# Kernel tuning notes

Hardware: AMD Instinct MI355X
Metric: run time of the kernel (lower is better)

## Reference

```python
import jax, jax.numpy as jnp
import numpy as np

B, K, D, C = 8192, 16, 1024, 512


def setup_inputs() -> dict:
    key = jax.random.key(0)
    k1, k2, k3, k4, k5 = jax.random.split(key, 5)
    concepts = jax.random.normal(k1, (B, K, D), dtype=jnp.float32)
    slot_ids = jax.random.randint(k2, (B,), 0, K)
    labels = jax.random.randint(k3, (B,), 0, C)
    # per-slot Linear(concept_dim -> num_classes): weight (K, C, D), bias (K, C)
    W = jax.random.normal(k4, (K, C, D), dtype=jnp.float32) / np.sqrt(D).astype(np.float32)
    bias = jax.random.normal(k5, (K, C), dtype=jnp.float32) * 0.01
    return {"concepts": concepts, "slot_ids": slot_ids, "labels": labels, "W": W, "bias": bias}


def reference(concepts, slot_ids, labels, W, bias):
    # Each example b uses slot s=slot_ids[b]: logits = concepts[b, s, :] @ W[s].T + bias[s].
    # Vectorized as K batched GEMMs over the slot axis, then gather the relevant row.
    logits = jnp.einsum('bkd,kcd->bkc', concepts, W) + bias  # (B, K, C)
    logp = jax.nn.log_softmax(logits, axis=-1)
    bidx = jnp.arange(concepts.shape[0])
    ce = -logp[bidx, slot_ids, labels]  # per-example cross entropy (B,)
    nK = W.shape[0]
    counts = jax.ops.segment_sum(jnp.ones_like(ce), slot_ids, num_segments=nK)
    sums = jax.ops.segment_sum(ce, slot_ids, num_segments=nK)
    means = sums / jnp.maximum(counts, 1.0)          # per-slot mean CE (= F.cross_entropy per group)
    present = counts > 0
    n_present = jnp.maximum(jnp.sum(present), 1)     # torch: count of unique slots, max(count,1)
    return jnp.sum(jnp.where(present, means, 0.0)) / n_present
```

## Files before the change

### kernel.cpp

```cpp
#include <hip/hip_runtime.h>
#include <hip/hip_bf16.h>

#define B_N 8192
#define K_N 16
#define D_N 1024
#define C_N 512
#define BM  32

typedef __bf16 bf16x8 __attribute__((ext_vector_type(8)));
typedef float  f32x4  __attribute__((ext_vector_type(4)));
typedef float  f32x4v __attribute__((ext_vector_type(4)));
typedef unsigned int u32x4 __attribute__((ext_vector_type(4)));

static __device__ __forceinline__ unsigned short f2bf(float f) {
    union { float f; unsigned int u; } x; x.f = f;
    unsigned int r = x.u + 0x7FFFu + ((x.u >> 16) & 1u);
    return (unsigned short)(r >> 16);
}

static __device__ __forceinline__ bf16x8 load_bf8(const unsigned short* p) {
    union { u32x4 u; bf16x8 v; } t;
    t.u = *(const u32x4*)p;
    return t.v;
}

static __device__ __forceinline__ bf16x8 zero_bf8() {
    union { u32x4 u; bf16x8 v; } t;
    u32x4 z = {0u, 0u, 0u, 0u};
    t.u = z;
    return t.v;
}

__global__ __launch_bounds__(256) void prep(const int* __restrict__ slot_ids,
                                            const int* __restrict__ labels,
                                            int* __restrict__ counts,
                                            int* __restrict__ offsets_g,
                                            float* __restrict__ ce_sums,
                                            int* __restrict__ order_rows,
                                            int* __restrict__ lab_g) {
    __shared__ int h[256][K_N];
    __shared__ int g[256][K_N];
    __shared__ int soff[K_N];
    int t = threadIdx.x;
    int ids[32];

#pragma unroll
    for (int s = 0; s < K_N; ++s) h[t][s] = 0;
#pragma unroll
    for (int i = 0; i < 32; ++i) {
        int b = i * 256 + t;
        int s = slot_ids[b];
        ids[i] = s;
        h[t][s]++;
    }
#pragma unroll
    for (int s = 0; s < K_N; ++s) g[t][s] = h[t][s];
    __syncthreads();

    for (int d = 1; d < 256; d <<= 1) {
        int v[K_N];
        if (t >= d) {
#pragma unroll
            for (int s = 0; s < K_N; ++s) v[s] = h[t - d][s];
        }
        __syncthreads();
        if (t >= d) {
#pragma unroll
            for (int s = 0; s < K_N; ++s) h[t][s] += v[s];
        }
        __syncthreads();
    }

    if (t == 0) {
        int a = 0;
#pragma unroll
        for (int s = 0; s < K_N; ++s) {
            int c = h[255][s];
            counts[s] = c;
            soff[s] = a;
            offsets_g[s] = a;
            a += c;
        }
    }
    if (t < K_N) ce_sums[t] = 0.f;
    __syncthreads();

#pragma unroll
    for (int s = 0; s < K_N; ++s) h[t][s] = soff[s] + h[t][s] - g[t][s];

#pragma unroll
    for (int i = 0; i < 32; ++i) {
        int b = i * 256 + t;
        int s = ids[i];
        int idx = h[t][s]++;
        order_rows[idx] = b * K_N + s;
        lab_g[idx] = labels[b];
    }
}

__global__ void convw(const float* __restrict__ W, unsigned short* __restrict__ Wb) {
    int i = (blockIdx.x * 256 + threadIdx.x) * 8;
    f32x4v a = *(const f32x4v*)(W + i);
    f32x4v b = *(const f32x4v*)(W + i + 4);
    u32x4 o;
    o[0] = (unsigned)f2bf(a[0]) | ((unsigned)f2bf(a[1]) << 16);
    o[1] = (unsigned)f2bf(a[2]) | ((unsigned)f2bf(a[3]) << 16);
    o[2] = (unsigned)f2bf(b[0]) | ((unsigned)f2bf(b[1]) << 16);
    o[3] = (unsigned)f2bf(b[2]) | ((unsigned)f2bf(b[3]) << 16);
    *(u32x4*)(Wb + i) = o;
}

__global__ __launch_bounds__(256) void gemm_ce(
        const float* __restrict__ concepts, const unsigned short* __restrict__ Wb,
        const float* __restrict__ bias, const int* __restrict__ counts,
        const int* __restrict__ offsets, const int* __restrict__ order_rows,
        const int* __restrict__ lab_g, float* __restrict__ ce_sums) {
    int s = blockIdx.y;
    int cnt = counts[s];
    int row0 = blockIdx.x * BM;
    if (row0 >= cnt) return;
    int nrows = min(BM, cnt - row0);
    int base = offsets[s];

    int tid = threadIdx.x;
    int wave = tid >> 6, lane = tid & 63;
    int col = lane & 15, quad = lane >> 4;
    int c0 = wave * 128;

    __shared__ int srow[BM];
    if (tid < BM)
        srow[tid] = order_rows[base + row0 + min(tid, nrows - 1)];
    __syncthreads();

    f32x4 acc[2][8];
    f32x4 zf = {0.f, 0.f, 0.f, 0.f};
#pragma unroll
    for (int m = 0; m < 2; ++m)
#pragma unroll
        for (int t = 0; t < 8; ++t) acc[m][t] = zf;

    const float* aptr[2];
    bool avalid[2];
#pragma unroll
    for (int m = 0; m < 2; ++m) {
        int lr = m * 16 + col;
        avalid[m] = lr < nrows;
        aptr[m] = concepts + (size_t)srow[lr] * D_N + quad * 8;
    }
    const unsigned short* bptr = Wb + ((size_t)s * C_N + c0 + col) * D_N + quad * 8;

    for (int k = 0; k < D_N; k += 32) {
        bf16x8 af[2];
#pragma unroll
        for (int m = 0; m < 2; ++m) {
            f32x4 a0 = *(const f32x4*)(aptr[m] + k);
            f32x4 a1 = *(const f32x4*)(aptr[m] + k + 4);
            bf16x8 v;
            v[0] = (__bf16)a0[0]; v[1] = (__bf16)a0[1];
            v[2] = (__bf16)a0[2]; v[3] = (__bf16)a0[3];
            v[4] = (__bf16)a1[0]; v[5] = (__bf16)a1[1];
            v[6] = (__bf16)a1[2]; v[7] = (__bf16)a1[3];
            af[m] = avalid[m] ? v : zero_bf8();
        }
        bf16x8 bfr[8];
#pragma unroll
        for (int t = 0; t < 8; ++t)
            bfr[t] = load_bf8(bptr + (size_t)t * 16 * D_N + k);
#pragma unroll
        for (int m = 0; m < 2; ++m)
#pragma unroll
            for (int t = 0; t < 8; ++t)
                acc[m][t] = __builtin_amdgcn_mfma_f32_16x16x32_bf16(af[m], bfr[t], acc[m][t], 0, 0, 0);
    }

    __shared__ float smax[4][BM];
    __shared__ float ssum[4][BM];
    __shared__ float gmax[BM];
    __shared__ float slab[BM];

#pragma unroll
    for (int t = 0; t < 8; ++t) {
        float bv = bias[(size_t)s * C_N + c0 + t * 16 + col];
#pragma unroll
        for (int m = 0; m < 2; ++m)
#pragma unroll
            for (int r = 0; r < 4; ++r) acc[m][t][r] += bv;
    }

#pragma unroll
    for (int m = 0; m < 2; ++m)
#pragma unroll
        for (int r = 0; r < 4; ++r) {
            float v = acc[m][0][r];
#pragma unroll
            for (int t = 1; t < 8; ++t) v = fmaxf(v, acc[m][t][r]);
            v = fmaxf(v, __shfl_xor(v, 1, 64));
            v = fmaxf(v, __shfl_xor(v, 2, 64));
            v = fmaxf(v, __shfl_xor(v, 4, 64));
            v = fmaxf(v, __shfl_xor(v, 8, 64));
            if (col == 0) smax[wave][m * 16 + quad * 4 + r] = v;
        }
    __syncthreads();
    if (tid < BM)
        gmax[tid] = fmaxf(fmaxf(smax[0][tid], smax[1][tid]),
                          fmaxf(smax[2][tid], smax[3][tid]));
    __syncthreads();

#pragma unroll
    for (int m = 0; m < 2; ++m)
#pragma unroll
        for (int r = 0; r < 4; ++r) {
            int row = m * 16 + quad * 4 + r;
            float gm = gmax[row];
            int lab = (row < nrows) ? lab_g[base + row0 + row] : -1;
            float sv = 0.f;
#pragma unroll
            for (int t = 0; t < 8; ++t) {
                float x = acc[m][t][r];
                sv += __expf(x - gm);
                if (c0 + t * 16 + col == lab) slab[row] = x;
            }
            sv += __shfl_xor(sv, 1, 64);
            sv += __shfl_xor(sv, 2, 64);
            sv += __shfl_xor(sv, 4, 64);
            sv += __shfl_xor(sv, 8, 64);
            if (col == 0) ssum[wave][row] = sv;
        }
    __syncthreads();

    if (wave == 0) {
        float ce = 0.f;
        if (lane < nrows) {
            float gs = ssum[0][lane] + ssum[1][lane] + ssum[2][lane] + ssum[3][lane];
            ce = gmax[lane] + __logf(gs) - slab[lane];
        }
        ce += __shfl_xor(ce, 1, 64);
        ce += __shfl_xor(ce, 2, 64);
        ce += __shfl_xor(ce, 4, 64);
        ce += __shfl_xor(ce, 8, 64);
        ce += __shfl_xor(ce, 16, 64);
        ce += __shfl_xor(ce, 32, 64);
        if (lane == 0) atomicAdd(&ce_sums[s], ce);
    }
}

__global__ void finalize(const int* __restrict__ counts, const float* __restrict__ ce_sums,
                         float* __restrict__ out) {
    if (threadIdx.x == 0 && blockIdx.x == 0) {
        float tot = 0.f; int np = 0;
        for (int s = 0; s < K_N; ++s) {
            int c = counts[s];
            if (c > 0) { tot += ce_sums[s] / (float)c; np++; }
        }
        out[0] = tot / (float)(np > 0 ? np : 1);
    }
}

extern "C" void kernel_launch(void* const* d_in, const int* in_sizes, int n_in,
                              void* d_out, int out_size, void* d_ws, size_t ws_size,
                              hipStream_t stream) {
    const float* concepts = (const float*)d_in[0];
    const int*   slot_ids = (const int*)d_in[1];
    const int*   labels   = (const int*)d_in[2];
    const float* W        = (const float*)d_in[3];
    const float* bias     = (const float*)d_in[4];
    float* out = (float*)d_out;

    char* ws = (char*)d_ws;
    int*   counts     = (int*)(ws + 0);
    int*   offsets    = (int*)(ws + 64);
    float* ce_sums    = (float*)(ws + 192);
    int*   order_rows = (int*)(ws + 256);
    int*   lab_g      = (int*)(ws + 256 + 4 * B_N);
    unsigned short* Wb = (unsigned short*)(ws + 131072);

    convw<<<(K_N * C_N * D_N) / (256 * 8), 256, 0, stream>>>(W, Wb);
    prep<<<1, 256, 0, stream>>>(slot_ids, labels, counts, offsets, ce_sums, order_rows, lab_g);
    gemm_ce<<<dim3(B_N / BM, K_N), 256, 0, stream>>>(concepts, Wb, bias, counts, offsets,
                                                     order_rows, lab_g, ce_sums);
    finalize<<<1, 1, 0, stream>>>(counts, ce_sums, out);
}
```

Measured before the change: 750.6 us.

## Use compact 1D slot-block grid, halve row tile, fuse setup and finalize

Merges the weight conversion and the slot histogram/sort into one launch, and folds the final reduction into the GEMM kernel through a last-block-done atomic counter. The GEMM grid changes from a sparse (B/BM, K) grid, where most blocks exit early, to a compact 1D list of per-slot blocks found via prefix block bases. BM drops from 32 to 16, so each block does one MFMA row tile and there are more blocks. This removes launch overhead and idle blocks, but each block now reuses every bf16 weight fragment it loads for half as many rows.

Result: faster. 733.6 us (-2.3%).

```diff
diff --git a/kernel.cpp b/kernel.cpp
--- a/kernel.cpp
+++ b/kernel.cpp
@@ -5,11 +5,12 @@
 #define K_N 16
 #define D_N 1024
 #define C_N 512
-#define BM  32
+#define BM  16
+#define CONVW_BLOCKS ((K_N * C_N * D_N) / (256 * 8))
+#define GEMM_BLOCKS  (B_N / BM + K_N)
 
 typedef __bf16 bf16x8 __attribute__((ext_vector_type(8)));
 typedef float  f32x4  __attribute__((ext_vector_type(4)));
-typedef float  f32x4v __attribute__((ext_vector_type(4)));
 typedef unsigned int u32x4 __attribute__((ext_vector_type(4)));
 
 static __device__ __forceinline__ unsigned short f2bf(float f) {
@@ -31,18 +32,32 @@
     return t.v;
 }
 
-__global__ __launch_bounds__(256) void prep(const int* __restrict__ slot_ids,
-                                            const int* __restrict__ labels,
-                                            int* __restrict__ counts,
-                                            int* __restrict__ offsets_g,
-                                            float* __restrict__ ce_sums,
-                                            int* __restrict__ order_rows,
-                                            int* __restrict__ lab_g) {
+__global__ __launch_bounds__(256) void setup(
+        const float* __restrict__ W, unsigned short* __restrict__ Wb,
+        const int* __restrict__ slot_ids, const int* __restrict__ labels,
+        int* __restrict__ counts, int* __restrict__ offsets_g,
+        int* __restrict__ blk_base, int* __restrict__ done,
+        float* __restrict__ ce_sums, int* __restrict__ order_rows,
+        int* __restrict__ lab_g) {
     __shared__ int h[256][K_N];
-    __shared__ int g[256][K_N];
     __shared__ int soff[K_N];
     int t = threadIdx.x;
+
+    if (blockIdx.x < CONVW_BLOCKS) {
+        size_t i = ((size_t)blockIdx.x * 256 + t) * 8;
+        f32x4 a = *(const f32x4*)(W + i);
+        f32x4 b = *(const f32x4*)(W + i + 4);
+        u32x4 o;
+        o[0] = (unsigned)f2bf(a[0]) | ((unsigned)f2bf(a[1]) << 16);
+        o[1] = (unsigned)f2bf(a[2]) | ((unsigned)f2bf(a[3]) << 16);
+        o[2] = (unsigned)f2bf(b[0]) | ((unsigned)f2bf(b[1]) << 16);
+        o[3] = (unsigned)f2bf(b[2]) | ((unsigned)f2bf(b[3]) << 16);
+        *(u32x4*)(Wb + i) = o;
+        return;
+    }
+
     int ids[32];
+    int own[K_N];
 
 #pragma unroll
     for (int s = 0; s < K_N; ++s) h[t][s] = 0;
@@ -54,7 +69,7 @@
         h[t][s]++;
     }
 #pragma unroll
-    for (int s = 0; s < K_N; ++s) g[t][s] = h[t][s];
+    for (int s = 0; s < K_N; ++s) own[s] = h[t][s];
     __syncthreads();
 
     for (int d = 1; d < 256; d <<= 1) {
@@ -72,7 +87,8 @@
     }
 
     if (t == 0) {
-        int a = 0;
+        int a = 0, nb = 0;
+        blk_base[0] = 0;
 #pragma unroll
         for (int s = 0; s < K_N; ++s) {
             int c = h[255][s];
@@ -80,145 +96,123 @@
             soff[s] = a;
             offsets_g[s] = a;
             a += c;
-        }
+            nb += (c + BM - 1) / BM;
+            blk_base[s + 1] = nb;
+        }
+        *done = 0;
     }
     if (t < K_N) ce_sums[t] = 0.f;
     __syncthreads();
 
 #pragma unroll
-    for (int s = 0; s < K_N; ++s) h[t][s] = soff[s] + h[t][s] - g[t][s];
+    for (int s = 0; s < K_N; ++s) own[s] = soff[s] + h[t][s] - own[s];
 
 #pragma unroll
     for (int i = 0; i < 32; ++i) {
         int b = i * 256 + t;
         int s = ids[i];
-        int idx = h[t][s]++;
+        int idx = own[s]++;
         order_rows[idx] = b * K_N + s;
         lab_g[idx] = labels[b];
     }
-}
-
-__global__ void convw(const float* __restrict__ W, unsigned short* __restrict__ Wb) {
-    int i = (blockIdx.x * 256 + threadIdx.x) * 8;
-    f32x4v a = *(const f32x4v*)(W + i);
-    f32x4v b = *(const f32x4v*)(W + i + 4);
-    u32x4 o;
-    o[0] = (unsigned)f2bf(a[0]) | ((unsigned)f2bf(a[1]) << 16);
-    o[1] = (unsigned)f2bf(a[2]) | ((unsigned)f2bf(a[3]) << 16);
-    o[2] = (unsigned)f2bf(b[0]) | ((unsigned)f2bf(b[1]) << 16);
-    o[3] = (unsigned)f2bf(b[2]) | ((unsigned)f2bf(b[3]) << 16);
-    *(u32x4*)(Wb + i) = o;
 }
 
 __global__ __launch_bounds__(256) void gemm_ce(
         const float* __restrict__ concepts, const unsigned short* __restrict__ Wb,
         const float* __restrict__ bias, const int* __restrict__ counts,
-        const int* __restrict__ offsets, const int* __restrict__ order_rows,
-        const int* __restrict__ lab_g, float* __restrict__ ce_sums) {
-    int s = blockIdx.y;
-    int cnt = counts[s];
-    int row0 = blockIdx.x * BM;
-    if (row0 >= cnt) return;
-    int nrows = min(BM, cnt - row0);
-    int base = offsets[s];
-
+        const int* __restrict__ offsets, const int* __restrict__ blk_base,
+        const int* __restrict__ order_rows, const int* __restrict__ lab_g,
+        int* __restrict__ done, float* __restrict__ ce_sums,
+        float* __restrict__ out) {
+    __shared__ int srow[BM];
+    __shared__ float smax[4][BM];
+    __shared__ float ssum[4][BM];
+    __shared__ float gmax[BM];
+    __shared__ float slab[BM];
+
+    int bid = blockIdx.x;
+    int nb_total = blk_base[K_N];
     int tid = threadIdx.x;
-    int wave = tid >> 6, lane = tid & 63;
-    int col = lane & 15, quad = lane >> 4;
-    int c0 = wave * 128;
-
-    __shared__ int srow[BM];
-    if (tid < BM)
-        srow[tid] = order_rows[base + row0 + min(tid, nrows - 1)];
-    __syncthreads();
-
-    f32x4 acc[2][8];
-    f32x4 zf = {0.f, 0.f, 0.f, 0.f};
-#pragma unroll
-    for (int m = 0; m < 2; ++m)
-#pragma unroll
-        for (int t = 0; t < 8; ++t) acc[m][t] = zf;
-
-    const float* aptr[2];
-    bool avalid[2];
-#pragma unroll
-    for (int m = 0; m < 2; ++m) {
-        int lr = m * 16 + col;
-        avalid[m] = lr < nrows;
-        aptr[m] = concepts + (size_t)srow[lr] * D_N + quad * 8;
-    }
-    const unsigned short* bptr = Wb + ((size_t)s * C_N + c0 + col) * D_N + quad * 8;
-
-    for (int k = 0; k < D_N; k += 32) {
-        bf16x8 af[2];
-#pragma unroll
-        for (int m = 0; m < 2; ++m) {
-            f32x4 a0 = *(const f32x4*)(aptr[m] + k);
-            f32x4 a1 = *(const f32x4*)(aptr[m] + k + 4);
+
+    if (bid < nb_total) {
+        int s = 0;
+        while (s < K_N - 1 && bid >= blk_base[s + 1]) ++s;
+        int cnt = counts[s];
+        int base = offsets[s];
+        int row0 = (bid - blk_base[s]) * BM;
+        int nrows = min(BM, cnt - row0);
+
+        int wave = tid >> 6, lane = tid & 63;
+        int col = lane & 15, quad = lane >> 4;
+        int c0 = wave * 128;
+
+        if (tid < BM)
+            srow[tid] = order_rows[base + row0 + min(tid, nrows - 1)];
+        __syncthreads();
+
+        f32x4 acc[8];
+        f32x4 zf = {0.f, 0.f, 0.f, 0.f};
+#pragma unroll
+        for (int t8 = 0; t8 < 8; ++t8) acc[t8] = zf;
+
+        bool avalid = col < nrows;
+        const float* aptr = concepts + (size_t)srow[col] * D_N + quad * 8;
+        const unsigned short* bptr = Wb + ((size_t)s * C_N + c0 + col) * D_N + quad * 8;
+
+        for (int k = 0; k < D_N; k += 32) {
+            f32x4 a0 = *(const f32x4*)(aptr + k);
+            f32x4 a1 = *(const f32x4*)(aptr + k + 4);
             bf16x8 v;
             v[0] = (__bf16)a0[0]; v[1] = (__bf16)a0[1];
             v[2] = (__bf16)a0[2]; v[3] = (__bf16)a0[3];
             v[4] = (__bf16)a1[0]; v[5] = (__bf16)a1[1];
             v[6] = (__bf16)a1[2]; v[7] = (__bf16)a1[3];
-            af[m] = avalid[m] ? v : zero_bf8();
-        }
-        bf16x8 bfr[8];
-#pragma unroll
-        for (int t = 0; t < 8; ++t)
-            bfr[t] = load_bf8(bptr + (size_t)t * 16 * D_N + k);
-#pragma unroll
-        for (int m = 0; m < 2; ++m)
-#pragma unroll
-            for (int t = 0; t < 8; ++t)
-                acc[m][t] = __builtin_amdgcn_mfma_f32_16x16x32_bf16(af[m], bfr[t], acc[m][t], 0, 0, 0);
-    }
-
-    __shared__ float smax[4][BM];
-    __shared__ float ssum[4][BM];
-    __shared__ float gmax[BM];
-    __shared__ float slab[BM];
-
-#pragma unroll
-    for (int t = 0; t < 8; ++t) {
-        float bv = bias[(size_t)s * C_N + c0 + t * 16 + col];
-#pragma unroll
-        for (int m = 0; m < 2; ++m)
-#pragma unroll
-            for (int r = 0; r < 4; ++r) acc[m][t][r] += bv;
-    }
-
-#pragma unroll
-    for (int m = 0; m < 2; ++m)
+            bf16x8 af = avalid ? v : zero_bf8();
+            bf16x8 bfr[8];
+#pragma unroll
+            for (int t8 = 0; t8 < 8; ++t8)
+                bfr[t8] = load_bf8(bptr + (size_t)t8 * 16 * D_N + k);
+#pragma unroll
+            for (int t8 = 0; t8 < 8; ++t8)
+                acc[t8] = __builtin_amdgcn_mfma_f32_16x16x32_bf16(af, bfr[t8], acc[t8], 0, 0, 0);
+        }
+
+#pragma unroll
+        for (int t8 = 0; t8 < 8; ++t8) {
+            float bv = bias[(size_t)s * C_N + c0 + t8 * 16 + col];
+#pragma unroll
+            for (int r = 0; r < 4; ++r) acc[t8][r] += bv;
+        }
+
 #pragma unroll
         for (int r = 0; r < 4; ++r) {
-            float v = acc[m][0][r];
-#pragma unroll
-            for (int t = 1; t < 8; ++t) v = fmaxf(v, acc[m][t][r]);
+            int row = quad * 4 + r;
+            float v = acc[0][r];
+#pragma unroll
+            for (int t8 = 1; t8 < 8; ++t8) v = fmaxf(v, acc[t8][r]);
             v = fmaxf(v, __shfl_xor(v, 1, 64));
             v = fmaxf(v, __shfl_xor(v, 2, 64));
             v = fmaxf(v, __shfl_xor(v, 4, 64));
             v = fmaxf(v, __shfl_xor(v, 8, 64));
-            if (col == 0) smax[wave][m * 16 + quad * 4 + r] = v;
-        }
-    __syncthreads();
-    if (tid < BM)
-        gmax[tid] = fmaxf(fmaxf(smax[0][tid], smax[1][tid]),
-                          fmaxf(smax[2][tid], smax[3][tid]));
-    __syncthreads();
-
-#pragma unroll
-    for (int m = 0; m < 2; ++m)
+            if (col == 0) smax[wave][row] = v;
+        }
+        __syncthreads();
+        if (tid < BM)
+            gmax[tid] = fmaxf(fmaxf(smax[0][tid], smax[1][tid]),
+                              fmaxf(smax[2][tid], smax[3][tid]));
+        __syncthreads();
+
 #pragma unroll
         for (int r = 0; r < 4; ++r) {
-            int row = m * 16 + quad * 4 + r;
+            int row = quad * 4 + r;
             float gm = gmax[row];
             int lab = (row < nrows) ? lab_g[base + row0 + row] : -1;
             float sv = 0.f;
 #pragma unroll
-            for (int t = 0; t < 8; ++t) {
-                float x = acc[m][t][r];
+            for (int t8 = 0; t8 < 8; ++t8) {
+                float x = acc[t8][r];
                 sv += __expf(x - gm);
-                if (c0 + t * 16 + col == lab) slab[row] = x;
+                if (c0 + t8 * 16 + col == lab) slab[row] = x;
             }
             sv += __shfl_xor(sv, 1, 64);
             sv += __shfl_xor(sv, 2, 64);
@@ -226,33 +220,39 @@
             sv += __shfl_xor(sv, 8, 64);
             if (col == 0) ssum[wave][row] = sv;
         }
+        __syncthreads();
+
+        if (wave == 0) {
+            float ce = 0.f;
+            if (lane < nrows) {
+                float gs = ssum[0][lane] + ssum[1][lane] + ssum[2][lane] + ssum[3][lane];
+                ce = gmax[lane] + __logf(gs) - slab[lane];
+            }
+            ce += __shfl_xor(ce, 1, 64);
+            ce += __shfl_xor(ce, 2, 64);
+            ce += __shfl_xor(ce, 4, 64);
+            ce += __shfl_xor(ce, 8, 64);
+            ce += __shfl_xor(ce, 16, 64);
+            ce += __shfl_xor(ce, 32, 64);
+            if (lane == 0) atomicAdd(&ce_sums[s], ce);
+        }
+    }
+
     __syncthreads();
-
-    if (wave == 0) {
-        float ce = 0.f;
-        if (lane < nrows) {
-            float gs = ssum[0][lane] + ssum[1][lane] + ssum[2][lane] + ssum[3][lane];
-            ce = gmax[lane] + __logf(gs) - slab[lane];
-        }
-        ce += __shfl_xor(ce, 1, 64);
-        ce += __shfl_xor(ce, 2, 64);
-        ce += __shfl_xor(ce, 4, 64);
-        ce += __shfl_xor(ce, 8, 64);
-        ce += __shfl_xor(ce, 16, 64);
-        ce += __shfl_xor(ce, 32, 64);
-        if (lane == 0) atomicAdd(&ce_sums[s], ce);
-    }
-}
-
-__global__ void finalize(const int* __restrict__ counts, const float* __restrict__ ce_sums,
-                         float* __restrict__ out) {
-    if (threadIdx.x == 0 && blockIdx.x == 0) {
-        float tot = 0.f; int np = 0;
-        for (int s = 0; s < K_N; ++s) {
-            int c = counts[s];
-            if (c > 0) { tot += ce_sums[s] / (float)c; np++; }
-        }
-        out[0] = tot / (float)(np > 0 ? np : 1);
+    if (tid == 0) {
+        __threadfence();
+        int old = atomicAdd(done, 1);
+        if (old == (int)gridDim.x - 1) {
+            float tot = 0.f; int np = 0;
+            for (int s2 = 0; s2 < K_N; ++s2) {
+                int c = counts[s2];
+                if (c > 0) {
+                    float cs = atomicAdd(&ce_sums[s2], 0.0f);
+                    tot += cs / (float)c; np++;
+                }
+            }
+            out[0] = tot / (float)(np > 0 ? np : 1);
+        }
     }
 }
 
@@ -269,14 +269,15 @@
     char* ws = (char*)d_ws;
     int*   counts     = (int*)(ws + 0);
     int*   offsets    = (int*)(ws + 64);
-    float* ce_sums    = (float*)(ws + 192);
-    int*   order_rows = (int*)(ws + 256);
-    int*   lab_g      = (int*)(ws + 256 + 4 * B_N);
+    int*   blk_base   = (int*)(ws + 128);
+    int*   done       = (int*)(ws + 256);
+    float* ce_sums    = (float*)(ws + 320);
+    int*   order_rows = (int*)(ws + 512);
+    int*   lab_g      = (int*)(ws + 512 + 4 * B_N);
     unsigned short* Wb = (unsigned short*)(ws + 131072);
 
-    convw<<<(K_N * C_N * D_N) / (256 * 8), 256, 0, stream>>>(W, Wb);
-    prep<<<1, 256, 0, stream>>>(slot_ids, labels, counts, offsets, ce_sums, order_rows, lab_g);
-    gemm_ce<<<dim3(B_N / BM, K_N), 256, 0, stream>>>(concepts, Wb, bias, counts, offsets,
-                                                     order_rows, lab_g, ce_sums);
-    finalize<<<1, 1, 0, stream>>>(counts, ce_sums, out);
-}
+    setup<<<CONVW_BLOCKS + 1, 256, 0, stream>>>(W, Wb, slot_ids, labels, counts, offsets,
+                                                blk_base, done, ce_sums, order_rows, lab_g);
+    gemm_ce<<<GEMM_BLOCKS, 256, 0, stream>>>(concepts, Wb, bias, counts, offsets, blk_base,
+                                             order_rows, lab_g, done, ce_sums, out);
+}
```
